# Optimization experiments

Hardware: AMD Instinct MI355X
Metric: run time of the kernel (lower is better)

Reference implementation:

```python
import jax, jax.numpy as jnp
import numpy as np

THETA = 10000.0
CLASS_RANGE = 24
CLASS_INTERVAL = 4
ROPE_H1 = (0.0, float(CLASS_INTERVAL))                       # (0, 4)
ROPE_H2 = (float(CLASS_RANGE - CLASS_INTERVAL), float(CLASS_RANGE))  # (20, 24)
ROPE_BAK = CLASS_RANGE // 2                                  # 12
EPS = 1e-8


def normalize_and_scale(v, src, tgt):
    s_min, s_max = src
    t_min, t_max = tgt
    return (v - s_min) / (s_max - s_min + EPS) * (t_max - t_min) + t_min


def rope_1d(x, positions):
    # x: (B, H, S, D); positions: (S,)
    D = x.shape[-1]
    inv_freq = 1.0 / (THETA ** (jnp.arange(0, D, 2, dtype=jnp.float32) / D))
    f = positions[:, None] * inv_freq[None, :]          # (S, D/2)
    cos, sin = jnp.cos(f), jnp.sin(f)
    x1, x2 = x[..., 0::2], x[..., 1::2]
    o1 = x1 * cos - x2 * sin
    o2 = x1 * sin + x2 * cos
    return jnp.stack([o1, o2], axis=-1).reshape(x.shape)


def setup_inputs() -> dict:
    key = jax.random.key(0)
    ks = jax.random.split(key, 10)
    B, N_t, S, C = 1, 21, 1560, 2048
    N_a, A = 32, 768
    return {
        "x": jax.random.normal(ks[0], (B, N_t * S, C), jnp.float32),
        "encoder_hidden_states": jax.random.normal(ks[1], (B * N_t, N_a, A), jnp.float32),
        "x_ref_attn_map": jax.random.uniform(ks[2], (2, N_t * S), jnp.float32),
        "q_w": jax.random.normal(ks[3], (C, C), jnp.float32) * 0.02,
        "q_b": jax.random.normal(ks[4], (C,), jnp.float32) * 0.02,
        "kv_w": jax.random.normal(ks[5], (2 * C, A), jnp.float32) * 0.02,
        "kv_b": jax.random.normal(ks[6], (2 * C,), jnp.float32) * 0.02,
        "proj_w": jax.random.normal(ks[7], (C, C), jnp.float32) * 0.02,
        "proj_b": jax.random.normal(ks[8], (C,), jnp.float32) * 0.02,
        "N_t": 21,
    }


def reference(x, encoder_hidden_states, x_ref_attn_map, q_w, q_b, kv_w, kv_b, proj_w, proj_b, N_t):
    B, N_total, C = x.shape
    S = N_total // N_t
    H = 32
    D = C // H
    BNt = B * N_t

    # q projection: (B*N_t, S, H, D)
    xr = x.reshape(BNt, S, C)
    q = (jnp.einsum('bsc,oc->bso', xr, q_w) + q_b).reshape(BNt, S, H, D)

    # multi-person RoPE positions for queries
    h1_max, h1_min = x_ref_attn_map[0].max(), x_ref_attn_map[0].min()
    h2_max, h2_min = x_ref_attn_map[1].max(), x_ref_attn_map[1].min()
    human1 = normalize_and_scale(x_ref_attn_map[0], (h1_min, h1_max), ROPE_H1)
    human2 = normalize_and_scale(x_ref_attn_map[1], (h2_min, h2_max), ROPE_H2)
    back = jnp.full((x_ref_attn_map.shape[1],), ROPE_BAK, dtype=human1.dtype)
    max_idx = jnp.argmax(x_ref_attn_map, axis=0)         # (N_t*S,), values in {0,1}
    nmap = jnp.stack([human1, human2, back], axis=1)     # (N_t*S, 3)
    normalized_pos = jnp.take_along_axis(nmap, max_idx[:, None], axis=1)[:, 0]

    qf = q.reshape(B, N_t * S, H, D).transpose(0, 2, 1, 3)   # (B, H, N_t*S, D)
    qf = rope_1d(qf, normalized_pos)
    q = qf.transpose(0, 2, 1, 3).reshape(BNt, S, H, D)

    # kv projection: (B*N_t, N_a, 2, H, D)
    N_a = encoder_hidden_states.shape[1]
    kv = jnp.einsum('bac,oc->bao', encoder_hidden_states, kv_w) + kv_b
    kv = kv.reshape(BNt, N_a, 2, H, D)
    k, v = kv[:, :, 0], kv[:, :, 1]

    # k RoPE with per-half constant positions
    half = N_a // 2
    per_frame = jnp.concatenate([
        jnp.full((half,), (ROPE_H1[0] + ROPE_H1[1]) / 2, jnp.float32),
        jnp.full((N_a - half,), (ROPE_H2[0] + ROPE_H2[1]) / 2, jnp.float32),
    ])
    encoder_pos = jnp.tile(per_frame, N_t)
    kf = k.reshape(B, N_t * N_a, H, D).transpose(0, 2, 1, 3)
    kf = rope_1d(kf, encoder_pos)
    k = kf.transpose(0, 2, 1, 3).reshape(BNt, N_a, H, D)

    # per-frame windowed cross-attention (non-causal)
    scale = 1.0 / jnp.sqrt(jnp.asarray(D, jnp.float32))
    scores = jnp.einsum('bshd,bahd->bhsa', q, k) * scale     # (BNt, H, S, N_a)
    probs = jax.nn.softmax(scores, axis=-1)
    out = jnp.einsum('bhsa,bahd->bshd', probs, v)            # (BNt, S, H, D)

    out = out.reshape(BNt, S, C)
    out = jnp.einsum('bsc,oc->bso', out, proj_w) + proj_b
    return out.reshape(B, N_t * S, C)
```

## Files before the change

### kernel.cpp

```cpp
#include <hip/hip_runtime.h>

typedef short bf16x8 __attribute__((ext_vector_type(8)));
typedef float f32x4 __attribute__((ext_vector_type(4)));

#define LN10000_32 0.2878231406211853f

__device__ __forceinline__ unsigned short f2bf(float f) {
  union { float f; unsigned int u; } v; v.f = f;
  unsigned int r = v.u + 0x7fffu + ((v.u >> 16) & 1u);
  return (unsigned short)(r >> 16);
}
__device__ __forceinline__ float bf2f(unsigned short h) {
  union { unsigned int u; float f; } v; v.u = ((unsigned int)h) << 16;
  return v.f;
}

__device__ __forceinline__ void stage16(const unsigned short* g, unsigned short* lds_base, int lane) {
#if __has_builtin(__builtin_amdgcn_global_load_lds)
  (void)lane;
  __builtin_amdgcn_global_load_lds((const __attribute__((address_space(1))) void*)g,
                                   (__attribute__((address_space(3))) void*)lds_base,
                                   16, 0, 0);
#else
  *(bf16x8*)((char*)lds_base + lane * 16) = *(const bf16x8*)g;
#endif
}

__global__ void minmax_kernel(const float* __restrict__ xmap, float* __restrict__ mm) {
  __shared__ float red[4][256];
  int t = threadIdx.x;
  float mn0 = 3.4e38f, mx0 = -3.4e38f, mn1 = 3.4e38f, mx1 = -3.4e38f;
  for (int i = t; i < 32760; i += 256) {
    float a = xmap[i];          mn0 = fminf(mn0, a); mx0 = fmaxf(mx0, a);
    float b = xmap[32760 + i];  mn1 = fminf(mn1, b); mx1 = fmaxf(mx1, b);
  }
  red[0][t] = mn0; red[1][t] = mx0; red[2][t] = mn1; red[3][t] = mx1;
  __syncthreads();
  for (int s = 128; s > 0; s >>= 1) {
    if (t < s) {
      red[0][t] = fminf(red[0][t], red[0][t + s]);
      red[1][t] = fmaxf(red[1][t], red[1][t + s]);
      red[2][t] = fminf(red[2][t], red[2][t + s]);
      red[3][t] = fmaxf(red[3][t], red[3][t + s]);
    }
    __syncthreads();
  }
  if (t == 0) { mm[0] = red[0][0]; mm[1] = red[1][0]; mm[2] = red[2][0]; mm[3] = red[3][0]; }
}

__global__ void pos_table_kernel(const float* __restrict__ xmap, const float* __restrict__ mm,
                                 float2* __restrict__ tab) {
  int n = blockIdx.x * 256 + threadIdx.x;
  if (n >= 32760) return;
  float m0 = xmap[n], m1 = xmap[32760 + n];
  float pos;
  if (m1 > m0) pos = (m1 - mm[2]) / (mm[3] - mm[2] + 1e-8f) * 4.0f + 20.0f;
  else         pos = (m0 - mm[0]) / (mm[1] - mm[0] + 1e-8f) * 4.0f;
  #pragma unroll
  for (int j = 0; j < 32; j++) {
    float invf = __expf(-(float)j * LN10000_32);
    float f = pos * invf;
    float s, c;
    sincosf(f, &s, &c);
    tab[(long)n * 32 + j] = make_float2(c, s);
  }
}

__global__ void cast_x_kernel(const float* __restrict__ src, unsigned short* __restrict__ dst) {
  int r = blockIdx.x;
  int c = threadIdx.x * 8;
  bf16x8 o;
  if (r < 32760) {
    const float4* s = (const float4*)(src + (long)r * 2048 + c);
    float4 a = s[0], b = s[1];
    o[0] = (short)f2bf(a.x); o[1] = (short)f2bf(a.y); o[2] = (short)f2bf(a.z); o[3] = (short)f2bf(a.w);
    o[4] = (short)f2bf(b.x); o[5] = (short)f2bf(b.y); o[6] = (short)f2bf(b.z); o[7] = (short)f2bf(b.w);
  } else {
    #pragma unroll
    for (int t = 0; t < 8; t++) o[t] = 0;
  }
  *(bf16x8*)(dst + (long)r * 2048 + c) = o;
}

__global__ void cast_flat_kernel(const float* __restrict__ src, unsigned short* __restrict__ dst, long n8) {
  long i = (long)blockIdx.x * 256 + threadIdx.x;
  if (i >= n8) return;
  const float4* s = (const float4*)(src + i * 8);
  float4 a = s[0], b = s[1];
  bf16x8 o;
  o[0] = (short)f2bf(a.x); o[1] = (short)f2bf(a.y); o[2] = (short)f2bf(a.z); o[3] = (short)f2bf(a.w);
  o[4] = (short)f2bf(b.x); o[5] = (short)f2bf(b.y); o[6] = (short)f2bf(b.z); o[7] = (short)f2bf(b.w);
  *(bf16x8*)(dst + i * 8) = o;
}

__global__ void cast_ehs_kernel(const float* __restrict__ src, unsigned short* __restrict__ dst) {
  int idx = blockIdx.x * 256 + threadIdx.x;
  int r = idx / 96, c = (idx % 96) * 8;
  bf16x8 o;
  if (r < 672) {
    const float4* s = (const float4*)(src + (long)r * 768 + c);
    float4 a = s[0], b = s[1];
    o[0] = (short)f2bf(a.x); o[1] = (short)f2bf(a.y); o[2] = (short)f2bf(a.z); o[3] = (short)f2bf(a.w);
    o[4] = (short)f2bf(b.x); o[5] = (short)f2bf(b.y); o[6] = (short)f2bf(b.z); o[7] = (short)f2bf(b.w);
  } else {
    #pragma unroll
    for (int t = 0; t < 8; t++) o[t] = 0;
  }
  *(bf16x8*)(dst + (long)r * 768 + c) = o;
}

template <int OUTF>
__global__ __launch_bounds__(256, 2)
void gemm_bt(const unsigned short* __restrict__ A, const unsigned short* __restrict__ B,
             const float* __restrict__ bias, void* __restrict__ C,
             int M, int N, int K, int M_valid) {
  __shared__ unsigned short As[128 * 32];
  __shared__ unsigned short Bs[128 * 32];
  int mt = blockIdx.x, nt = blockIdx.y;
  const int m0 = mt * 128;
  const int n0 = nt * 128;
  const int tid = threadIdx.x;
  const int wave = tid >> 6;
  const int lane = tid & 63;
  const int wr = wave >> 1, wc = wave & 1;
  const int lrow = lane >> 2, lcol = lane & 3;

  f32x4 acc[4][4];
  #pragma unroll
  for (int i = 0; i < 4; i++)
    #pragma unroll
    for (int j = 0; j < 4; j++) acc[i][j] = (f32x4){0.f, 0.f, 0.f, 0.f};

  const unsigned short* gA = A + (long)(m0 + wave * 32 + lrow) * K + lcol * 8;
  const unsigned short* gB = B + (long)(n0 + wave * 32 + lrow) * K + lcol * 8;
  unsigned short* lA0 = &As[wave * 1024];
  unsigned short* lA1 = &As[wave * 1024 + 512];
  unsigned short* lB0 = &Bs[wave * 1024];
  unsigned short* lB1 = &Bs[wave * 1024 + 512];

  for (int k0 = 0; k0 < K; k0 += 32) {
    stage16(gA + k0, lA0, lane);
    stage16(gA + k0 + 16 * K, lA1, lane);
    stage16(gB + k0, lB0, lane);
    stage16(gB + k0 + 16 * K, lB1, lane);
    __syncthreads();
    bf16x8 af[4], bfr[4];
    const int kq = (lane >> 4) * 8;
    const int rr = lane & 15;
    #pragma unroll
    for (int mi = 0; mi < 4; mi++) af[mi] = *(const bf16x8*)&As[(wr * 64 + mi * 16 + rr) * 32 + kq];
    #pragma unroll
    for (int ni = 0; ni < 4; ni++) bfr[ni] = *(const bf16x8*)&Bs[(wc * 64 + ni * 16 + rr) * 32 + kq];
    #pragma unroll
    for (int mi = 0; mi < 4; mi++)
      #pragma unroll
      for (int ni = 0; ni < 4; ni++)
        acc[mi][ni] = __builtin_amdgcn_mfma_f32_16x16x32_bf16(af[mi], bfr[ni], acc[mi][ni], 0, 0, 0);
    __syncthreads();
  }

  const int colL = lane & 15, rq = (lane >> 4) * 4;
  #pragma unroll
  for (int mi = 0; mi < 4; mi++) {
    #pragma unroll
    for (int ni = 0; ni < 4; ni++) {
      int col = n0 + wc * 64 + ni * 16 + colL;
      float bv = bias[col];
      #pragma unroll
      for (int r = 0; r < 4; r++) {
        int row = m0 + wr * 64 + mi * 16 + rq + r;
        if (row < M_valid) {
          float v = acc[mi][ni][r] + bv;
          if (OUTF) ((float*)C)[(long)row * N + col] = v;
          else      ((unsigned short*)C)[(long)row * N + col] = f2bf(v);
        }
      }
    }
  }
}

template <int OUTF>
__global__ __launch_bounds__(512, 2)
void gemm256(const unsigned short* __restrict__ A, const unsigned short* __restrict__ B,
             const float* __restrict__ bias, void* __restrict__ C,
             int K, int N, int M_valid) {
  extern __shared__ __align__(16) unsigned short lds[];
  const int NT = K >> 6;
  const int NI = NT >> 1;
  const int orig = blockIdx.x;
  const int cpx = (int)gridDim.x >> 3;
  const int wgid = (orig & 7) * cpx + (orig >> 3);
  const int nt = wgid & 7;
  const int mt = wgid >> 3;
  const int m0 = mt << 8, n0 = nt << 8;
  const int tid = threadIdx.x;
  const int w = tid >> 6, l = tid & 63;
  const int wr = w >> 2, wc = w & 3;
  const int i = l & 15, kq = l >> 4;

  const int swz0 = ((kq) ^ (i & 7)) * 8;
  const int swz1 = ((4 + kq) ^ (i & 7)) * 8;
  const int aoff = wr * 8192 + i * 64;
  const int boff = 16384 + (wc >> 1) * 8192 + (wc & 1) * 4096 + i * 64;

  const int srow = l >> 3;
  const int scb = ((l & 7) ^ srow) * 8;
  const int sdst = w * 512;
  const unsigned short* Asrc = A + (long)(m0 + w * 8 + srow) * K + scb;
  const unsigned short* Bsrc = B + (long)(n0 + w * 8 + srow) * K + scb;

  f32x4 acc[8][4];
  #pragma unroll
  for (int a_ = 0; a_ < 8; a_++)
    #pragma unroll
    for (int b_ = 0; b_ < 4; b_++) acc[a_][b_] = (f32x4){0.f, 0.f, 0.f, 0.f};

  bf16x8 a[4][2], b[4][2];

#define BAR __builtin_amdgcn_s_barrier()
#define VM4 asm volatile("s_waitcnt vmcnt(4)" ::: "memory")
#define VM0 asm volatile("s_waitcnt vmcnt(0)" ::: "memory")

#define STG_A(T, h) do { \
    const unsigned short* s_ = Asrc + (long)((h) * 128) * K + (T) * 64; \
    unsigned short* d_ = lds + (((T) & 1) << 15) + ((h) << 13) + sdst; \
    stage16(s_, d_, l); \
    stage16(s_ + (long)64 * K, d_ + 4096, l); \
  } while (0)
#define STG_B(T, h) do { \
    const unsigned short* s_ = Bsrc + (long)((h) * 128) * K + (T) * 64; \
    unsigned short* d_ = lds + (((T) & 1) << 15) + 16384 + ((h) << 13) + sdst; \
    stage16(s_, d_, l); \
    stage16(s_ + (long)64 * K, d_ + 4096, l); \
  } while (0)

#define RD_A(bufo, mh) do { \
    const unsigned short* p_ = lds + (bufo) + aoff + (mh) * 4096; \
    a[0][0] = *(const bf16x8*)(p_ + swz0);        a[0][1] = *(const bf16x8*)(p_ + swz1); \
    a[1][0] = *(const bf16x8*)(p_ + 1024 + swz0); a[1][1] = *(const bf16x8*)(p_ + 1024 + swz1); \
    a[2][0] = *(const bf16x8*)(p_ + 2048 + swz0); a[2][1] = *(const bf16x8*)(p_ + 2048 + swz1); \
    a[3][0] = *(const bf16x8*)(p_ + 3072 + swz0); a[3][1] = *(const bf16x8*)(p_ + 3072 + swz1); \
  } while (0)
#define RD_B(bufo, nf) do { \
    const unsigned short* p_ = lds + (bufo) + boff + (nf) * 1024; \
    b[nf][0] = *(const bf16x8*)(p_ + swz0); \
    b[nf][1] = *(const bf16x8*)(p_ + swz1); \
  } while (0)

#define MMQ(AB, N0, N1) do { \
    __builtin_amdgcn_s_setprio(1); \
    _Pragma("unroll") \
    for (int q_ = 0; q_ < 4; q_++) { \
      acc[(AB) + q_][N0] = __builtin_amdgcn_mfma_f32_16x16x32_bf16(a[q_][0], b[N0][0], acc[(AB) + q_][N0], 0, 0, 0); \
      acc[(AB) + q_][N1] = __builtin_amdgcn_mfma_f32_16x16x32_bf16(a[q_][0], b[N1][0], acc[(AB) + q_][N1], 0, 0, 0); \
    } \
    _Pragma("unroll") \
    for (int q_ = 0; q_ < 4; q_++) { \
      acc[(AB) + q_][N0] = __builtin_amdgcn_mfma_f32_16x16x32_bf16(a[q_][1], b[N0][1], acc[(AB) + q_][N0], 0, 0, 0); \
      acc[(AB) + q_][N1] = __builtin_amdgcn_mfma_f32_16x16x32_bf16(a[q_][1], b[N1][1], acc[(AB) + q_][N1], 0, 0, 0); \
    } \
    __builtin_amdgcn_s_setprio(0); \
  } while (0)

#define GEMM_ITER(T0v, T1v, FULL, GATEP4, GATEP8) do { \
    const int T0_ = (T0v), T1_ = (T1v); \
     RD_A(0, 0); RD_B(0, 0); RD_B(0, 1); STG_B(T1_, 1); BAR; MMQ(0, 0, 1); BAR; \
     RD_B(0, 2); RD_B(0, 3); STG_A(T1_, 1); BAR; MMQ(0, 2, 3); BAR; \
     RD_A(0, 1); if (FULL) { STG_B(T0_ + 2, 0); } BAR; MMQ(4, 2, 3); BAR; \
     if (FULL) { STG_A(T0_ + 2, 0); } GATEP4; BAR; MMQ(4, 0, 1); BAR; \
     RD_A(32768, 0); RD_B(32768, 0); RD_B(32768, 1); if (FULL) { STG_B(T0_ + 2, 1); } BAR; MMQ(0, 0, 1); BAR; \
     RD_B(32768, 2); RD_B(32768, 3); if (FULL) { STG_A(T0_ + 2, 1); } BAR; MMQ(0, 2, 3); BAR; \
     RD_A(32768, 1); if (FULL) { STG_B(T1_ + 2, 0); } BAR; MMQ(4, 2, 3); BAR; \
     if (FULL) { STG_A(T1_ + 2, 0); } GATEP8; BAR; MMQ(4, 0, 1); BAR; \
  } while (0)

  STG_B(0, 0); STG_A(0, 0); STG_B(0, 1); STG_A(0, 1);
  STG_B(1, 0); STG_A(1, 0);
  VM4; BAR;

  for (int j = 0; j < NI - 1; ++j) {
    GEMM_ITER(2 * j, 2 * j + 1, 1, VM4, VM4);
  }
  GEMM_ITER(NT - 2, NT - 1, 0, VM0, (void)0);

#undef GEMM_ITER
#undef MMQ
#undef RD_B
#undef RD_A
#undef STG_B
#undef STG_A
#undef VM0
#undef VM4
#undef BAR

  #pragma unroll
  for (int nf = 0; nf < 4; nf++) {
    int col = n0 + wc * 64 + nf * 16 + i;
    float bv = bias[col];
    #pragma unroll
    for (int mf = 0; mf < 8; mf++) {
      int rowb = m0 + wr * 128 + mf * 16 + kq * 4;
      #pragma unroll
      for (int r = 0; r < 4; r++) {
        int row = rowb + r;
        if (row < M_valid) {
          float v = acc[mf][nf][r] + bv;
          if (OUTF) ((float*)C)[(long)row * N + col] = v;
          else      ((unsigned short*)C)[(long)row * N + col] = f2bf(v);
        }
      }
    }
  }
}

__global__ __launch_bounds__(256)
void attn_mfma(const unsigned short* __restrict__ kv, unsigned short* __restrict__ q,
               const float2* __restrict__ tab) {
  __shared__ unsigned short Vt[64 * 40];
  __shared__ unsigned short Pl[4][32 * 40];
  const int bh = blockIdx.y;
  const int b = bh >> 5, h = bh & 31;
  const int tid = threadIdx.x;
  const int w = tid >> 6, l = tid & 63;
  const int i16 = l & 15, kq = l >> 4;

  {
    int a = tid & 31, d0 = (tid >> 5) * 8;
    const unsigned short* vp = kv + ((long)(b * 32 + a)) * 4096 + 2048 + h * 64 + d0;
    bf16x8 v = *(const bf16x8*)vp;
    #pragma unroll
    for (int j = 0; j < 8; j++) Vt[(d0 + j) * 40 + a] = (unsigned short)v[j];
  }

  bf16x8 bk[2][2];
  #pragma unroll
  for (int nf = 0; nf < 2; nf++) {
    int a = nf * 16 + i16;
    float pos = (a < 16) ? 2.0f : 22.0f;
    const unsigned short* kp = kv + ((long)(b * 32 + a)) * 4096 + h * 64;
    #pragma unroll
    for (int ks = 0; ks < 2; ks++) {
      int d0 = ks * 32 + kq * 8;
      bf16x8 v = *(const bf16x8*)(kp + d0);
      bf16x8 o;
      #pragma unroll
      for (int t = 0; t < 4; t++) {
        float invf = __expf(-(float)((d0 >> 1) + t) * LN10000_32);
        float f = pos * invf, s_, c_;
        sincosf(f, &s_, &c_);
        float x1 = bf2f((unsigned short)v[2 * t]), x2 = bf2f((unsigned short)v[2 * t + 1]);
        o[2 * t]     = (short)f2bf(x1 * c_ - x2 * s_);
        o[2 * t + 1] = (short)f2bf(x1 * s_ + x2 * c_);
      }
      bk[nf][ks] = o;
    }
  }

  __syncthreads();

  const int s0 = blockIdx.x * 128 + w * 32;
  bf16x8 aq[2][2];
  #pragma unroll
  for (int mf = 0; mf < 2; mf++) {
    int srow = s0 + mf * 16 + i16;
    int sc_ = srow < 1560 ? srow : 1559;
    long row = (long)b * 1560 + sc_;
    const unsigned short* qp = q + row * 2048 + h * 64;
    const float2* trow = tab + row * 32;
    #pragma unroll
    for (int ks = 0; ks < 2; ks++) {
      int d0 = ks * 32 + kq * 8;
      bf16x8 v = *(const bf16x8*)(qp + d0);
      float4 t0 = *(const float4*)&trow[(d0 >> 1)];
      float4 t1 = *(const float4*)&trow[(d0 >> 1) + 2];
      float cs[4] = {t0.x, t0.z, t1.x, t1.z};
      float sn[4] = {t0.y, t0.w, t1.y, t1.w};
      bf16x8 o;
      #pragma unroll
      for (int t = 0; t < 4; t++) {
        float x1 = bf2f((unsigned short)v[2 * t]), x2 = bf2f((unsigned short)v[2 * t + 1]);
        o[2 * t]     = (short)f2bf(x1 * cs[t] - x2 * sn[t]);
        o[2 * t + 1] = (short)f2bf(x1 * sn[t] + x2 * cs[t]);
      }
      aq[mf][ks] = o;
    }
  }

  f32x4 sfr[2][2];
  #pragma unroll
  for (int mf = 0; mf < 2; mf++)
    #pragma unroll
    for (int nf = 0; nf < 2; nf++) {
      f32x4 c = {0.f, 0.f, 0.f, 0.f};
      c = __builtin_amdgcn_mfma_f32_16x16x32_bf16(aq[mf][0], bk[nf][0], c, 0, 0, 0);
      c = __builtin_amdgcn_mfma_f32_16x16x32_bf16(aq[mf][1], bk[nf][1], c, 0, 0, 0);
      sfr[mf][nf] = c;
    }

  float inv_s[2][4];
  #pragma unroll
  for (int mf = 0; mf < 2; mf++) {
    #pragma unroll
    for (int r = 0; r < 4; r++) {
      float v0 = sfr[mf][0][r] * 0.125f;
      float v1 = sfr[mf][1][r] * 0.125f;
      float mx = fmaxf(v0, v1);
      #pragma unroll
      for (int m_ = 1; m_ < 16; m_ <<= 1) mx = fmaxf(mx, __shfl_xor(mx, m_));
      float e0 = __expf(v0 - mx), e1 = __expf(v1 - mx);
      float sm = e0 + e1;
      #pragma unroll
      for (int m_ = 1; m_ < 16; m_ <<= 1) sm += __shfl_xor(sm, m_);
      inv_s[mf][r] = 1.0f / sm;
      sfr[mf][0][r] = e0; sfr[mf][1][r] = e1;
    }
  }

  unsigned short* pl = &Pl[w][0];
  #pragma unroll
  for (int mf = 0; mf < 2; mf++)
    #pragma unroll
    for (int nf = 0; nf < 2; nf++)
      #pragma unroll
      for (int r = 0; r < 4; r++)
        pl[(mf * 16 + kq * 4 + r) * 40 + nf * 16 + i16] = f2bf(sfr[mf][nf][r]);

  bf16x8 pa[2];
  #pragma unroll
  for (int mf = 0; mf < 2; mf++)
    pa[mf] = *(const bf16x8*)&pl[(mf * 16 + i16) * 40 + kq * 8];
  bf16x8 vb[4];
  #pragma unroll
  for (int nf = 0; nf < 4; nf++)
    vb[nf] = *(const bf16x8*)&Vt[(nf * 16 + i16) * 40 + kq * 8];
  f32x4 ofr[2][4];
  #pragma unroll
  for (int mf = 0; mf < 2; mf++)
    #pragma unroll
    for (int nf = 0; nf < 4; nf++) {
      f32x4 c = {0.f, 0.f, 0.f, 0.f};
      ofr[mf][nf] = __builtin_amdgcn_mfma_f32_16x16x32_bf16(pa[mf], vb[nf], c, 0, 0, 0);
    }

  #pragma unroll
  for (int mf = 0; mf < 2; mf++) {
    #pragma unroll
    for (int r = 0; r < 4; r++) {
      int srow = s0 + mf * 16 + kq * 4 + r;
      if (srow < 1560) {
        unsigned short* op = q + ((long)b * 1560 + srow) * 2048 + h * 64;
        float inv = inv_s[mf][r];
        #pragma unroll
        for (int nf = 0; nf < 4; nf++)
          op[nf * 16 + i16] = f2bf(ofr[mf][nf][r] * inv);
      }
    }
  }
}

extern "C" void kernel_launch(void* const* d_in, const int* in_sizes, int n_in,
                              void* d_out, int out_size, void* d_ws, size_t ws_size,
                              hipStream_t stream) {
  const float* x      = (const float*)d_in[0];
  const float* ehs    = (const float*)d_in[1];
  const float* xmap   = (const float*)d_in[2];
  const float* q_w    = (const float*)d_in[3];
  const float* q_b    = (const float*)d_in[4];
  const float* kv_w   = (const float*)d_in[5];
  const float* kv_b   = (const float*)d_in[6];
  const float* proj_w = (const float*)d_in[7];
  const float* proj_b = (const float*)d_in[8];
  float* out = (float*)d_out;

  char* ws = (char*)d_ws;
  float*          mm    = (float*)(ws + 0);
  float2*         tab   = (float2*)(ws + 256);
  unsigned short* qbuf  = (unsigned short*)(ws + 8388864);
  unsigned short* kvbuf = (unsigned short*)(ws + 142606592);
  unsigned short* ehsb  = (unsigned short*)(ws + 148898048);
  unsigned short* qwb   = (unsigned short*)(ws + 150077696);
  unsigned short* kvwb  = (unsigned short*)(ws + 158466304);
  unsigned short* pwb   = (unsigned short*)(ws + 164757760);
  unsigned short* xb    = (unsigned short*)d_out;

  (void)hipFuncSetAttribute((const void*)gemm256<0>, hipFuncAttributeMaxDynamicSharedMemorySize, 131072);
  (void)hipFuncSetAttribute((const void*)gemm256<1>, hipFuncAttributeMaxDynamicSharedMemorySize, 131072);

  minmax_kernel<<<1, 256, 0, stream>>>(xmap, mm);
  pos_table_kernel<<<128, 256, 0, stream>>>(xmap, mm, tab);
  cast_x_kernel<<<32768, 256, 0, stream>>>(x, xb);
  cast_flat_kernel<<<2048, 256, 0, stream>>>(q_w, qwb, 524288);
  cast_flat_kernel<<<1536, 256, 0, stream>>>(kv_w, kvwb, 393216);
  cast_flat_kernel<<<2048, 256, 0, stream>>>(proj_w, pwb, 524288);
  cast_ehs_kernel<<<288, 256, 0, stream>>>(ehs, ehsb);

  gemm256<0><<<1024, 512, 131072, stream>>>(xb, qwb, q_b, qbuf, 2048, 2048, 32768);
  gemm_bt<0><<<dim3(6, 32), 256, 0, stream>>>(ehsb, kvwb, kv_b, kvbuf, 768, 4096, 768, 768);

  attn_mfma<<<dim3(13, 672), 256, 0, stream>>>(kvbuf, qbuf, tab);

  gemm256<1><<<1024, 512, 131072, stream>>>(qbuf, pwb, proj_b, out, 2048, 2048, 32760);
}
```

Before: 875.3 us.

## Precompute K RoPE once, merge weight casts, grid-stride x cast

K RoPE was recomputed in every attention block (13 s-tiles per batch-head). It now runs once in a separate kernel that rotates the kv buffer in place, so attention just loads the rotated K. The three weight-cast launches are merged into one kernel, and the x cast becomes a grid-stride loop over 2048 blocks. This adds one small kernel launch in exchange for removing redundant sincos work and two launches.

```diff
diff --git a/kernel.cpp b/kernel.cpp
--- a/kernel.cpp
+++ b/kernel.cpp
@@ -67,30 +67,41 @@
 }
 
 __global__ void cast_x_kernel(const float* __restrict__ src, unsigned short* __restrict__ dst) {
-  int r = blockIdx.x;
-  int c = threadIdx.x * 8;
-  bf16x8 o;
-  if (r < 32760) {
-    const float4* s = (const float4*)(src + (long)r * 2048 + c);
-    float4 a = s[0], b = s[1];
-    o[0] = (short)f2bf(a.x); o[1] = (short)f2bf(a.y); o[2] = (short)f2bf(a.z); o[3] = (short)f2bf(a.w);
-    o[4] = (short)f2bf(b.x); o[5] = (short)f2bf(b.y); o[6] = (short)f2bf(b.z); o[7] = (short)f2bf(b.w);
-  } else {
-    #pragma unroll
-    for (int t = 0; t < 8; t++) o[t] = 0;
-  }
-  *(bf16x8*)(dst + (long)r * 2048 + c) = o;
-}
-
-__global__ void cast_flat_kernel(const float* __restrict__ src, unsigned short* __restrict__ dst, long n8) {
+  const long total8 = (long)32768 * 256;
+  for (long g = (long)blockIdx.x * 256 + threadIdx.x; g < total8; g += (long)gridDim.x * 256) {
+    long r = g >> 8;
+    int c = (int)(g & 255) * 8;
+    bf16x8 o;
+    if (r < 32760) {
+      const float4* s = (const float4*)(src + r * 2048 + c);
+      float4 a = s[0], b = s[1];
+      o[0] = (short)f2bf(a.x); o[1] = (short)f2bf(a.y); o[2] = (short)f2bf(a.z); o[3] = (short)f2bf(a.w);
+      o[4] = (short)f2bf(b.x); o[5] = (short)f2bf(b.y); o[6] = (short)f2bf(b.z); o[7] = (short)f2bf(b.w);
+    } else {
+      #pragma unroll
+      for (int t = 0; t < 8; t++) o[t] = 0;
+    }
+    *(bf16x8*)(dst + r * 2048 + c) = o;
+  }
+}
+
+__global__ void cast_weights_kernel(const float* __restrict__ qw, const float* __restrict__ kvw,
+                                    const float* __restrict__ pw,
+                                    unsigned short* __restrict__ qwb, unsigned short* __restrict__ kvwb,
+                                    unsigned short* __restrict__ pwb) {
+  const long n0 = 524288, n1 = 917504, n2 = 1441792;
   long i = (long)blockIdx.x * 256 + threadIdx.x;
-  if (i >= n8) return;
-  const float4* s = (const float4*)(src + i * 8);
+  if (i >= n2) return;
+  const float* src; unsigned short* dst; long j;
+  if (i < n0)      { src = qw;  dst = qwb;  j = i; }
+  else if (i < n1) { src = kvw; dst = kvwb; j = i - n0; }
+  else             { src = pw;  dst = pwb;  j = i - n1; }
+  const float4* s = (const float4*)(src + j * 8);
   float4 a = s[0], b = s[1];
   bf16x8 o;
   o[0] = (short)f2bf(a.x); o[1] = (short)f2bf(a.y); o[2] = (short)f2bf(a.z); o[3] = (short)f2bf(a.w);
   o[4] = (short)f2bf(b.x); o[5] = (short)f2bf(b.y); o[6] = (short)f2bf(b.z); o[7] = (short)f2bf(b.w);
-  *(bf16x8*)(dst + i * 8) = o;
+  *(bf16x8*)(dst + j * 8) = o;
 }
 
 __global__ void cast_ehs_kernel(const float* __restrict__ src, unsigned short* __restrict__ dst) {
@@ -313,6 +324,28 @@
   }
 }
 
+__global__ void rope_k_kernel(unsigned short* __restrict__ kv) {
+  int r = blockIdx.x;
+  int c = threadIdx.x * 8;
+  float pos = ((r & 31) < 16) ? 2.0f : 22.0f;
+  unsigned short* p = kv + (long)r * 4096 + c;
+  bf16x8 v = *(const bf16x8*)p;
+  int jb = (c & 63) >> 1;
+  bf16x8 o;
+  #pragma unroll
+  for (int t = 0; t < 4; t++) {
+    float invf = __expf(-(float)(jb + t) * LN10000_32);
+    float f = pos * invf;
+    float s_, c_;
+    sincosf(f, &s_, &c_);
+    float x1 = bf2f((unsigned short)v[2 * t]);
+    float x2 = bf2f((unsigned short)v[2 * t + 1]);
+    o[2 * t]     = (short)f2bf(x1 * c_ - x2 * s_);
+    o[2 * t + 1] = (short)f2bf(x1 * s_ + x2 * c_);
+  }
+  *(bf16x8*)p = o;
+}
+
 __global__ __launch_bounds__(256)
 void attn_mfma(const unsigned short* __restrict__ kv, unsigned short* __restrict__ q,
                const float2* __restrict__ tab) {
@@ -335,25 +368,9 @@
   bf16x8 bk[2][2];
   #pragma unroll
   for (int nf = 0; nf < 2; nf++) {
-    int a = nf * 16 + i16;
-    float pos = (a < 16) ? 2.0f : 22.0f;
-    const unsigned short* kp = kv + ((long)(b * 32 + a)) * 4096 + h * 64;
-    #pragma unroll
-    for (int ks = 0; ks < 2; ks++) {
-      int d0 = ks * 32 + kq * 8;
-      bf16x8 v = *(const bf16x8*)(kp + d0);
-      bf16x8 o;
-      #pragma unroll
-      for (int t = 0; t < 4; t++) {
-        float invf = __expf(-(float)((d0 >> 1) + t) * LN10000_32);
-        float f = pos * invf, s_, c_;
-        sincosf(f, &s_, &c_);
-        float x1 = bf2f((unsigned short)v[2 * t]), x2 = bf2f((unsigned short)v[2 * t + 1]);
-        o[2 * t]     = (short)f2bf(x1 * c_ - x2 * s_);
-        o[2 * t + 1] = (short)f2bf(x1 * s_ + x2 * c_);
-      }
-      bk[nf][ks] = o;
-    }
+    const unsigned short* kp = kv + ((long)(b * 32 + nf * 16 + i16)) * 4096 + h * 64;
+    bk[nf][0] = *(const bf16x8*)(kp + kq * 8);
+    bk[nf][1] = *(const bf16x8*)(kp + 32 + kq * 8);
   }
 
   __syncthreads();
@@ -488,15 +505,15 @@
 
   minmax_kernel<<<1, 256, 0, stream>>>(xmap, mm);
   pos_table_kernel<<<128, 256, 0, stream>>>(xmap, mm, tab);
-  cast_x_kernel<<<32768, 256, 0, stream>>>(x, xb);
-  cast_flat_kernel<<<2048, 256, 0, stream>>>(q_w, qwb, 524288);
-  cast_flat_kernel<<<1536, 256, 0, stream>>>(kv_w, kvwb, 393216);
-  cast_flat_kernel<<<2048, 256, 0, stream>>>(proj_w, pwb, 524288);
+  cast_x_kernel<<<2048, 256, 0, stream>>>(x, xb);
+  cast_weights_kernel<<<5632, 256, 0, stream>>>(q_w, kv_w, proj_w, qwb, kvwb, pwb);
   cast_ehs_kernel<<<288, 256, 0, stream>>>(ehs, ehsb);
 
   gemm256<0><<<1024, 512, 131072, stream>>>(xb, qwb, q_b, qbuf, 2048, 2048, 32768);
   gemm_bt<0><<<dim3(6, 32), 256, 0, stream>>>(ehsb, kvwb, kv_b, kvbuf, 768, 4096, 768, 768);
 
+  rope_k_kernel<<<672, 256, 0, stream>>>(kvbuf);
+
   attn_mfma<<<dim3(13, 672), 256, 0, stream>>>(kvbuf, qbuf, tab);
 
   gemm256<1><<<1024, 512, 131072, stream>>>(qbuf, pwb, proj_b, out, 2048, 2048, 32760);
```

Result: no change. 876.4 us (+0.1%).
